# Kernel tuning notes

Measured on AMD Instinct MI355X. Metric: run time of the kernel, lower is better.

The kernel has to match this reference:

```python
import math
import jax, jax.numpy as jnp
import numpy as np

B, C, T = 2, 512, 2048
HEADS, NFREQS, NDECAY = 8, 4, 4
HD = C // HEADS  # head dim = 64


def _conv1x1(x, W, b):
    # pointwise Conv1d: W [out, in], b [out], x [B, in, T]
    return jnp.einsum('oi,bit->bot', W, x) + b[:, None]


def setup_inputs() -> dict:
    key = jax.random.key(0)
    ks = jax.random.split(key, 12)
    s = 1.0 / math.sqrt(C)
    inp = {
        'x': jax.random.normal(ks[0], (B, C, T), jnp.float32),
        'Wq': jax.random.normal(ks[1], (C, C), jnp.float32) * s,
        'bq': jnp.zeros((C,), jnp.float32),
        'Wk': jax.random.normal(ks[2], (C, C), jnp.float32) * s,
        'bk': jnp.zeros((C,), jnp.float32),
        'Wc': jax.random.normal(ks[3], (C, C), jnp.float32) * s,
        'bc': jnp.zeros((C,), jnp.float32),
        'Wqf': jax.random.normal(ks[4], (HEADS * NFREQS, C), jnp.float32) * s,
        'bqf': jnp.zeros((HEADS * NFREQS,), jnp.float32),
        # query_decay init: weight *= 0.01, bias = -2 (as in the torch module)
        'Wqd': jax.random.normal(ks[5], (HEADS * NDECAY, C), jnp.float32) * (s * 0.01),
        'bqd': jnp.full((HEADS * NDECAY,), -2.0, jnp.float32),
        'Wp': jax.random.normal(ks[6], (C, C), jnp.float32) * s,
        'bp': jnp.zeros((C,), jnp.float32),
    }
    return inp


def reference(x, Wq, bq, Wk, bk, Wc, bc, Wqf, bqf, Wqd, bqd, Wp, bp):
    Bx, Cx, Tx = x.shape
    idx = jnp.arange(Tx, dtype=x.dtype)
    delta = idx[:, None] - idx[None, :]  # [T, T]

    queries = _conv1x1(x, Wq, bq).reshape(Bx, HEADS, HD, Tx)
    keys = _conv1x1(x, Wk, bk).reshape(Bx, HEADS, HD, Tx)
    dots = jnp.einsum('bhct,bhcs->bhts', keys, queries) / math.sqrt(HD)

    # frequency bias
    periods = jnp.arange(1, NFREQS + 1, dtype=x.dtype)
    freq_kernel = jnp.cos(2 * math.pi * delta / periods[:, None, None])  # [f, T, T]
    freq_q = _conv1x1(x, Wqf, bqf).reshape(Bx, HEADS, NFREQS, Tx) / math.sqrt(NFREQS)
    dots = dots + jnp.einsum('fts,bhfs->bhts', freq_kernel, freq_q)

    # decay bias
    decays = jnp.arange(1, NDECAY + 1, dtype=x.dtype)
    decay_q = jax.nn.sigmoid(_conv1x1(x, Wqd, bqd).reshape(Bx, HEADS, NDECAY, Tx)) / 2
    decay_kernel = -decays[:, None, None] * jnp.abs(delta) / math.sqrt(NDECAY)
    dots = dots + jnp.einsum('fts,bhfs->bhts', decay_kernel, decay_q)

    # mask self-attention diagonal with -100, softmax over keys axis (t, dim=2)
    eye = jnp.eye(Tx, dtype=bool)
    dots = jnp.where(eye[None, None], jnp.asarray(-100.0, x.dtype), dots)
    weights = jax.nn.softmax(dots, axis=2)

    content = _conv1x1(x, Wc, bc).reshape(Bx, HEADS, HD, Tx)
    result = jnp.einsum('bhts,bhct->bhcs', weights, content).reshape(Bx, Cx, Tx)
    return x + _conv1x1(result, Wp, bp)
```

## Files before the change

kernel.cpp:

```cpp
#include <hip/hip_runtime.h>
#include <math.h>

#define T_SEQ 2048
#define C_DIM 512
#define B_SZ  2
#define NHEAD 8
#define HD    64
#define DP    128
#define MTOT  1600
#define NTILE 32

typedef unsigned short u16t;
typedef unsigned int   u32t;
typedef float f32x4 __attribute__((ext_vector_type(4)));
typedef short s16x8 __attribute__((ext_vector_type(8)));

__device__ __forceinline__ u32t pack2(float a, float b) {
    u32t r;
    asm("v_cvt_pk_bf16_f32 %0, %1, %2" : "=v"(r) : "v"(a), "v"(b));
    return r;
}
__device__ __forceinline__ u16t f2bf(float f) {
    union { float f; u32t u; } v; v.f = f;
    u32t r = v.u + 0x7fffu + ((v.u >> 16) & 1u);
    return (u16t)(r >> 16);
}
__device__ __forceinline__ float bf2f(u16t h) {
    union { u32t u; float f; } v; v.u = (u32t)h << 16; return v.f;
}

#define GLD16(g, l) __builtin_amdgcn_global_load_lds( \
    (const __attribute__((address_space(1))) u32t*)(g), \
    (__attribute__((address_space(3))) u32t*)(l), 16, 0, 0)

__global__ __launch_bounds__(256)
void wconv_kernel(const float* __restrict__ Wq, const float* __restrict__ Wk,
                  const float* __restrict__ Wc, const float* __restrict__ Wqf,
                  const float* __restrict__ Wqd, const float* __restrict__ Wp,
                  const float* __restrict__ bq, const float* __restrict__ bk,
                  const float* __restrict__ bc, const float* __restrict__ bqf,
                  const float* __restrict__ bqd,
                  u16t* __restrict__ Wcat, u16t* __restrict__ Wpbf,
                  float* __restrict__ biascat)
{
    int r = blockIdx.x, tid = threadIdx.x;
    if (r < MTOT) {
        const float* src;
        if (r < 512) src = Wq + (long long)r * C_DIM;
        else if (r < 1024) src = Wk + (long long)(r - 512) * C_DIM;
        else if (r < 1536) src = Wc + (long long)(r - 1024) * C_DIM;
        else if (r < 1568) src = Wqf + (long long)(r - 1536) * C_DIM;
        else src = Wqd + (long long)(r - 1568) * C_DIM;
        float2 v = *(const float2*)(src + tid * 2);
        *(u32t*)(Wcat + (long long)r * C_DIM + tid * 2) = pack2(v.x, v.y);
    } else if (r < MTOT + 512) {
        int rr = r - MTOT;
        float2 v = *(const float2*)(Wp + (long long)rr * C_DIM + tid * 2);
        *(u32t*)(Wpbf + (long long)rr * C_DIM + tid * 2) = pack2(v.x, v.y);
    } else {
        for (int i = tid; i < MTOT; i += 256) {
            float bv;
            if (i < 512) bv = bq[i];
            else if (i < 1024) bv = bk[i - 512];
            else if (i < 1536) bv = bc[i - 1024];
            else if (i < 1568) bv = bqf[i - 1536];
            else bv = bqd[i - 1568];
            biascat[i] = bv;
        }
    }
}

__global__ __launch_bounds__(256)
void xt_kernel(const float* __restrict__ x, u16t* __restrict__ xT)
{
    __shared__ float tile[64][65];
    int b = blockIdx.z, c0 = blockIdx.y * 64, t0 = blockIdx.x * 64;
    int tid = threadIdx.x;
    const float* xb = x + ((long long)b * C_DIM + c0) * T_SEQ + t0;
#pragma unroll
    for (int rr = 0; rr < 16; ++rr) {
        int row = rr * 4 + (tid >> 6);
        tile[row][tid & 63] = xb[(long long)row * T_SEQ + (tid & 63)];
    }
    __syncthreads();
    int tt = tid >> 2, cs = (tid & 3) * 16;
    u32t ov[8];
#pragma unroll
    for (int u = 0; u < 8; ++u)
        ov[u] = pack2(tile[cs + u * 2][tt], tile[cs + u * 2 + 1][tt]);
    u16t* dst = xT + ((long long)b * T_SEQ + t0 + tt) * C_DIM + c0 + cs;
    *(uint4*)(dst) = make_uint4(ov[0], ov[1], ov[2], ov[3]);
    *(uint4*)(dst + 8) = make_uint4(ov[4], ov[5], ov[6], ov[7]);
}

__global__ __launch_bounds__(256)
void gemm_kernel(const u16t* __restrict__ A, const u16t* __restrict__ Bm,
                 const float* __restrict__ biasv, const float* __restrict__ x,
                 u16t* __restrict__ Qbf, u16t* __restrict__ Kbf,
                 u16t* __restrict__ Vbf, float* __restrict__ fqd,
                 float* __restrict__ outp, int mode)
{
    __shared__ u16t At[2][64 * 64];
    __shared__ u16t Bt[2][64 * 64];
    int b = blockIdx.z, m0 = blockIdx.y * 64, n0 = blockIdx.x * 64;
    int tid = threadIdx.x, w = tid >> 6, lane = tid & 63;
    int l16 = lane & 15, l4 = lane >> 4;
    const u16t* Bb = Bm + (long long)b * T_SEQ * C_DIM;

    auto stage = [&](int kt, int bufi) {
        int k0 = kt * 64;
        const u16t* srcb = (w < 2) ? A + (long long)m0 * C_DIM + k0
                                   : Bb + (long long)n0 * C_DIM + k0;
        u16t* dstb = (w < 2) ? &At[bufi][0] : &Bt[bufi][0];
#pragma unroll
        for (int i = 0; i < 4; ++i) {
            int rb = (w & 1) * 32 + i * 8;
            int row = rb + (lane >> 3);
            int c = (lane & 7) ^ (row & 7);
            GLD16(srcb + (long long)row * C_DIM + c * 8, dstb + rb * 64);
        }
    };

    f32x4 acc[4] = {};
    stage(0, 0);
    for (int kt = 0; kt < 8; ++kt) {
        __syncthreads();
        if (kt < 7) stage(kt + 1, (kt + 1) & 1);
        const u16t* Ab = At[kt & 1];
        const u16t* Bb2 = Bt[kt & 1];
        int nl = w * 16 + l16;
#pragma unroll
        for (int kb = 0; kb < 2; ++kb) {
            s16x8 bf = *(const s16x8*)(&Bb2[nl * 64 + (((kb * 4 + l4) ^ (l16 & 7)) * 8)]);
#pragma unroll
            for (int rt = 0; rt < 4; ++rt) {
                s16x8 af = *(const s16x8*)(&At[kt & 1][(rt * 16 + l16) * 64 + (((kb * 4 + l4) ^ (l16 & 7)) * 8)]);
                acc[rt] = __builtin_amdgcn_mfma_f32_16x16x32_bf16(af, bf, acc[rt], 0, 0, 0);
            }
            (void)Ab;
        }
    }

    int n = n0 + w * 16 + l16;
    if (mode == 0) {
        if (m0 < 1024) {
            bool isQ = m0 < 512;
            int h = (isQ ? m0 : m0 - 512) >> 6;
            u16t* dst = (isQ ? Qbf : Kbf) + ((long long)(b * NHEAD + h) * T_SEQ + n) * DP;
            float sc = isQ ? 0.125f : 1.0f;
#pragma unroll
            for (int rt = 0; rt < 4; ++rt) {
                int d0 = (rt * 16 + l4 * 4) & 63;
                int m = m0 + rt * 16 + l4 * 4;
                float v0 = sc * (acc[rt][0] + biasv[m + 0]);
                float v1 = sc * (acc[rt][1] + biasv[m + 1]);
                float v2 = sc * (acc[rt][2] + biasv[m + 2]);
                float v3 = sc * (acc[rt][3] + biasv[m + 3]);
                *(uint2*)(dst + d0) = make_uint2(pack2(v0, v1), pack2(v2, v3));
            }
        } else if (m0 < 1536) {
#pragma unroll
            for (int rt = 0; rt < 4; ++rt)
#pragma unroll
                for (int j = 0; j < 4; ++j) {
                    int m = m0 + rt * 16 + l4 * 4 + j;
                    int c = m - 1024;
                    Vbf[((long long)b * C_DIM + c) * T_SEQ + n] = f2bf(acc[rt][j] + biasv[m]);
                }
        } else {
#pragma unroll
            for (int rt = 0; rt < 4; ++rt)
#pragma unroll
                for (int j = 0; j < 4; ++j) {
                    int m = m0 + rt * 16 + l4 * 4 + j;
                    fqd[((long long)b * 64 + (m - 1536)) * T_SEQ + n] = acc[rt][j] + biasv[m];
                }
        }
    } else {
#pragma unroll
        for (int rt = 0; rt < 4; ++rt)
#pragma unroll
            for (int j = 0; j < 4; ++j) {
                int m = m0 + rt * 16 + l4 * 4 + j;
                long long o = ((long long)b * C_DIM + m) * T_SEQ + n;
                outp[o] = acc[rt][j] + biasv[m] + x[o];
            }
    }
}

__global__ __launch_bounds__(256)
void kext_kernel(u16t* __restrict__ Kbf)
{
    int t = blockIdx.x * 256 + threadIdx.x;
    int bh = blockIdx.y;
    u32t e[4];
#pragma unroll
    for (int f = 0; f < 4; ++f) {
        float a = 2.0f * (float)t / (float)(f + 1);
        e[f] = pack2(cospif(a), sinpif(a));
    }
    u16t* row = Kbf + ((long long)bh * T_SEQ + t) * DP;
    *(uint4*)(row + 64) = make_uint4(e[0], e[1], e[2], e[3]);
    uint4 z = make_uint4(0, 0, 0, 0);
#pragma unroll
    for (int i = 0; i < 7; ++i) *(uint4*)(row + 72 + i * 8) = z;
}

__global__ __launch_bounds__(256)
void coef_kernel(const float* __restrict__ fqd, u16t* __restrict__ Qbf,
                 float* __restrict__ dcoef)
{
    int s = blockIdx.x * 256 + threadIdx.x;
    int bh = blockIdx.y, b = bh >> 3, h = bh & 7;
    const float* base = fqd + (long long)b * 64 * T_SEQ;
    float dsum = 0.f;
    u32t e[4];
#pragma unroll
    for (int f = 0; f < 4; ++f) {
        float fq = base[(long long)(h * 4 + f) * T_SEQ + s] * 0.5f;
        float zd = base[(long long)(32 + h * 4 + f) * T_SEQ + s];
        dsum += (float)(f + 1) / (1.f + __expf(-zd));
        float a = 2.0f * (float)s / (float)(f + 1);
        e[f] = pack2(fq * cospif(a), fq * sinpif(a));
    }
    u16t* row = Qbf + ((long long)bh * T_SEQ + s) * DP;
    *(uint4*)(row + 64) = make_uint4(e[0], e[1], e[2], e[3]);
    uint4 z = make_uint4(0, 0, 0, 0);
#pragma unroll
    for (int i = 0; i < 7; ++i) *(uint4*)(row + 72 + i * 8) = z;
    dcoef[(long long)bh * T_SEQ + s] = 0.25f * dsum;
}

__global__ __launch_bounds__(256)
void knorm_kernel(const u16t* __restrict__ Kbf, float* __restrict__ knorm)
{
    __shared__ float wmax[4];
    int tile = blockIdx.x, bh = blockIdx.y, tid = threadIdx.x;
    int row = tid >> 2, part = tid & 3;
    const u16t* rp = Kbf + ((long long)bh * T_SEQ + tile * 64 + row) * DP + part * 16;
    float ss = 0.f;
#pragma unroll
    for (int i = 0; i < 2; ++i) {
        s16x8 v = *(const s16x8*)(rp + i * 8);
#pragma unroll
        for (int e = 0; e < 8; ++e) { float f = bf2f((u16t)v[e]); ss += f * f; }
    }
    ss += __shfl_xor(ss, 1, 64);
    ss += __shfl_xor(ss, 2, 64);
    float nrm = sqrtf(ss + 4.1f);
#pragma unroll
    for (int off = 4; off < 64; off <<= 1) nrm = fmaxf(nrm, __shfl_xor(nrm, off, 64));
    if ((tid & 63) == 0) wmax[tid >> 6] = nrm;
    __syncthreads();
    if (tid == 0)
        knorm[bh * NTILE + tile] =
            fmaxf(fmaxf(wmax[0], wmax[1]), fmaxf(wmax[2], wmax[3]));
}

__global__ __launch_bounds__(256)
void attn_kernel(const u16t* __restrict__ Qbf, const u16t* __restrict__ Kbf,
                 const u16t* __restrict__ Vbf, const float* __restrict__ dcoef,
                 const float* __restrict__ knorm, u16t* __restrict__ Rt)
{
    __shared__ u16t Kt[2][64 * DP];
    __shared__ u16t Vt[2][64 * 64];
    __shared__ u16t Pl[4][16 * 64];
    __shared__ u32t voteLds[4];

    int bh = blockIdx.y, b = bh >> 3, h = bh & 7;
    int j0 = blockIdx.x;
    int s0 = j0 * 64;
    int tid = threadIdx.x, w = tid >> 6, lane = tid & 63;
    int l16 = lane & 15, l4 = lane >> 4;
    const u16t* Qg = Qbf + (long long)bh * T_SEQ * DP;
    const u16t* Kg = Kbf + (long long)bh * T_SEQ * DP;
    const u16t* Vg = Vbf + ((long long)b * C_DIM + h * HD) * T_SEQ;
    int sl = w * 16 + l16;
    int sg = s0 + sl;

    s16x8 qf[3];
#pragma unroll
    for (int kb = 0; kb < 3; ++kb)
        qf[kb] = *(const s16x8*)(Qg + (long long)sg * DP + kb * 32 + l4 * 8);
    float qn2 = 0.f;
#pragma unroll
    for (int kb = 0; kb < 3; ++kb)
#pragma unroll
        for (int e = 0; e < 8; ++e) { float f = bf2f((u16t)qf[kb][e]); qn2 += f * f; }
    qn2 += __shfl_xor(qn2, 16, 64);
    qn2 += __shfl_xor(qn2, 32, 64);
    float qn = sqrtf(qn2);
    float dc = dcoef[(long long)bh * T_SEQ + sg];
    float mrun = -1e30f, lrun = 0.f;
    f32x4 O4[4] = {};

    auto stageKV = [&](int tt0, int bufi) {
#pragma unroll
        for (int i = 0; i < 4; ++i) {
            int rb = w * 16 + i * 4;
            int row = rb + (lane >> 4);
            int c = (lane & 15) ^ (row & 7);
            GLD16(Kg + (long long)(tt0 + row) * DP + c * 8, &Kt[bufi][rb * DP]);
        }
#pragma unroll
        for (int i = 0; i < 2; ++i) {
            int cb = w * 16 + i * 8;
            int cc = cb + (lane >> 3);
            int tc = (lane & 7) ^ (cc & 7);
            GLD16(Vg + (long long)cc * T_SEQ + tt0 + tc * 8, &Vt[bufi][cb * 64]);
        }
    };

    auto compute_tile = [&](int tj, int bufi, bool diag) {
        const u16t* Kb = Kt[bufi];
        const u16t* Vb = Vt[bufi];
        int t0 = tj * 64;
        f32x4 sacc[4] = {};
#pragma unroll
        for (int kb = 0; kb < 3; ++kb)
#pragma unroll
            for (int rt = 0; rt < 4; ++rt) {
                s16x8 af = *(const s16x8*)(&Kb[(rt * 16 + l16) * DP + (((kb * 4 + l4) ^ (l16 & 7)) * 8)]);
                sacc[rt] = __builtin_amdgcn_mfma_f32_16x16x32_bf16(af, qf[kb], sacc[rt], 0, 0, 0);
            }
        float cm = mrun;
        float pv[4][4];
#pragma unroll
        for (int rt = 0; rt < 4; ++rt) {
            int tb = t0 + rt * 16 + l4 * 4;
#pragma unroll
            for (int j = 0; j < 4; ++j) {
                int t = tb + j;
                float v = sacc[rt][j] - fabsf((float)(t - sg)) * dc;
                if (diag && t == sg) v = -100.f;
                pv[rt][j] = v;
                cm = fmaxf(cm, v);
            }
        }
        cm = fmaxf(cm, __shfl_xor(cm, 16, 64));
        cm = fmaxf(cm, __shfl_xor(cm, 32, 64));
        if (__any(cm > mrun)) {
            float scale = __expf(mrun - cm);
            mrun = cm;
            lrun *= scale;
#pragma unroll
            for (int rt = 0; rt < 4; ++rt) O4[rt] *= scale;
        }
        float psum = 0.f;
#pragma unroll
        for (int rt = 0; rt < 4; ++rt)
#pragma unroll
            for (int j = 0; j < 4; ++j) {
                float p = __expf(pv[rt][j] - mrun);
                pv[rt][j] = p;
                psum += p;
            }
        psum += __shfl_xor(psum, 16, 64);
        psum += __shfl_xor(psum, 32, 64);
        lrun += psum;
#pragma unroll
        for (int rt = 0; rt < 4; ++rt) {
            int tl = rt * 16 + l4 * 4;
            int cp = (tl >> 3) ^ (l16 & 7);
            *(uint2*)(&Pl[w][l16 * 64 + cp * 8 + (tl & 7)]) =
                make_uint2(pack2(pv[rt][0], pv[rt][1]), pack2(pv[rt][2], pv[rt][3]));
        }
#pragma unroll
        for (int kb = 0; kb < 2; ++kb) {
            s16x8 pf = *(const s16x8*)(&Pl[w][l16 * 64 + (((kb * 4 + l4) ^ (l16 & 7)) * 8)]);
#pragma unroll
            for (int rt = 0; rt < 4; ++rt) {
                s16x8 vf = *(const s16x8*)(&Vb[(rt * 16 + l16) * 64 + (((kb * 4 + l4) ^ (l16 & 7)) * 8)]);
                O4[rt] = __builtin_amdgcn_mfma_f32_16x16x32_bf16(vf, pf, O4[rt], 0, 0, 0);
            }
        }
    };

    int seq[3]; int ns = 0;
    seq[ns++] = j0;
    if (j0 + 1 < NTILE) seq[ns++] = j0 + 1;
    if (j0 > 0) seq[ns++] = j0 - 1;
    stageKV(seq[0] * 64, 0);
    for (int i = 0; i < ns; ++i) {
        __syncthreads();
        if (i + 1 < ns) stageKV(seq[i + 1] * 64, (i + 1) & 1);
        compute_tile(seq[i], i & 1, seq[i] == j0);
    }

    u32t mask = 0;
    const float* knb = knorm + bh * NTILE;
    for (int j = 0; j < NTILE; ++j) {
        int d = j > j0 ? j - j0 : j0 - j;
        if (d <= 1) continue;
        float minD = (float)((d - 1) * 64 + 1);
        float bound = qn * knb[j] - dc * minD;
        if (__any(bound > mrun - 15.f)) mask |= 1u << j;
    }
    voteLds[w] = mask;
    __syncthreads();
    mask = voteLds[0] | voteLds[1] | voteLds[2] | voteLds[3];

    int parity = ns & 1;
    u32t rem = mask;
    if (rem) {
        int j = (int)__builtin_ctz(rem);
        stageKV(j * 64, parity);
        while (true) {
            rem &= rem - 1;
            __syncthreads();
            int nj = rem ? (int)__builtin_ctz(rem) : -1;
            if (nj >= 0) stageKV(nj * 64, parity ^ 1);
            compute_tile(j, parity, false);
            if (nj < 0) break;
            parity ^= 1;
            j = nj;
        }
    }

    __syncthreads();
    float inv = 1.f / lrun;
#pragma unroll
    for (int rt = 0; rt < 4; ++rt) {
        O4[rt] *= inv;
        int cb = rt * 16 + l4 * 4;
        int cp = (cb >> 3) ^ (sl & 7);
        *(uint2*)(&Kt[0][sl * 64 + cp * 8 + (cb & 7)]) =
            make_uint2(pack2(O4[rt][0], O4[rt][1]), pack2(O4[rt][2], O4[rt][3]));
    }
    __syncthreads();
    {
        int row = tid >> 2;
        int rsw = row & 7;
        u16t* dst = Rt + ((long long)b * T_SEQ + s0 + row) * C_DIM + h * HD;
#pragma unroll
        for (int i = 0; i < 2; ++i) {
            int cc = (tid & 3) + i * 4;
            uint4 v = *(const uint4*)(&Kt[0][row * 64 + ((cc ^ rsw) * 8)]);
            *(uint4*)(dst + cc * 8) = v;
        }
    }
}

extern "C" void kernel_launch(void* const* d_in, const int* in_sizes, int n_in,
                              void* d_out, int out_size, void* d_ws, size_t ws_size,
                              hipStream_t stream)
{
    const float* x   = (const float*)d_in[0];
    const float* Wq  = (const float*)d_in[1];
    const float* bq  = (const float*)d_in[2];
    const float* Wk  = (const float*)d_in[3];
    const float* bk  = (const float*)d_in[4];
    const float* Wc  = (const float*)d_in[5];
    const float* bc  = (const float*)d_in[6];
    const float* Wqf = (const float*)d_in[7];
    const float* bqf = (const float*)d_in[8];
    const float* Wqd = (const float*)d_in[9];
    const float* bqd = (const float*)d_in[10];
    const float* Wp  = (const float*)d_in[11];
    const float* bp  = (const float*)d_in[12];
    float* out = (float*)d_out;

    char* p = (char*)d_ws;
    u16t* Wcat = (u16t*)p;    p += (long long)MTOT * C_DIM * 2;
    u16t* Wpbf = (u16t*)p;    p += (long long)C_DIM * C_DIM * 2;
    float* biascat = (float*)p; p += MTOT * 4;
    u16t* xT = (u16t*)p;      p += (long long)B_SZ * T_SEQ * C_DIM * 2;
    u16t* Qbf = (u16t*)p;     p += (long long)16 * T_SEQ * DP * 2;
    u16t* Kbf = (u16t*)p;     p += (long long)16 * T_SEQ * DP * 2;
    u16t* Vbf = (u16t*)p;     p += (long long)B_SZ * C_DIM * T_SEQ * 2;
    float* fqd = (float*)p;   p += (long long)B_SZ * 64 * T_SEQ * 4;
    float* dcoef = (float*)p; p += (long long)16 * T_SEQ * 4;
    float* knorm = (float*)p; p += (long long)16 * NTILE * 4;
    u16t* Rt = (u16t*)p;      p += (long long)B_SZ * T_SEQ * C_DIM * 2;

    dim3 blk(256);
    hipLaunchKernelGGL(wconv_kernel, dim3(MTOT + 512 + 1), blk, 0, stream,
                       Wq, Wk, Wc, Wqf, Wqd, Wp, bq, bk, bc, bqf, bqd,
                       Wcat, Wpbf, biascat);
    hipLaunchKernelGGL(xt_kernel, dim3(T_SEQ / 64, C_DIM / 64, B_SZ), blk, 0, stream,
                       x, xT);
    hipLaunchKernelGGL(gemm_kernel, dim3(T_SEQ / 64, MTOT / 64, B_SZ), blk, 0, stream,
                       Wcat, xT, biascat, nullptr, Qbf, Kbf, Vbf, fqd, nullptr, 0);
    hipLaunchKernelGGL(kext_kernel, dim3(T_SEQ / 256, 16), blk, 0, stream, Kbf);
    hipLaunchKernelGGL(coef_kernel, dim3(T_SEQ / 256, 16), blk, 0, stream,
                       fqd, Qbf, dcoef);
    hipLaunchKernelGGL(knorm_kernel, dim3(NTILE, 16), blk, 0, stream, Kbf, knorm);
    hipLaunchKernelGGL(attn_kernel, dim3(T_SEQ / 64, 16), blk, 0, stream,
                       Qbf, Kbf, Vbf, dcoef, knorm, Rt);
    hipLaunchKernelGGL(gemm_kernel, dim3(T_SEQ / 64, C_DIM / 64, B_SZ), blk, 0, stream,
                       Wpbf, Rt, bp, (const float*)x, nullptr, nullptr, nullptr, nullptr,
                       out, 1);
}
```

Before: 63.78 us.

## Enlarge GEMM tiles, fuse Q/K extension kernels, add setprio and lazy softmax rescale

Replaces the 64x64 projection GEMM with a templated kernel that uses 128x128 tiles for the QKV/bias projection and 128x64 tiles for the output projection. Each wave now computes a 2D sub-tile, so every LDS fragment feeds more MFMAs, and the grid has fewer blocks. The last M tile overruns the 1600-row weight matrix, so its stores are guarded. The separate K-extension and coefficient kernels are merged into one launch that computes cos/sin once. The attention kernel gains s_setprio around its MFMA phases and rescales the online softmax only when the running max grows by more than 8, which trades some fp32 headroom for fewer rescale passes.

```diff
diff --git a/kernel.cpp b/kernel.cpp
--- a/kernel.cpp
+++ b/kernel.cpp
@@ -93,141 +93,165 @@
     *(uint4*)(dst + 8) = make_uint4(ov[4], ov[5], ov[6], ov[7]);
 }
 
+template<int BM, int BN, int MODE>
 __global__ __launch_bounds__(256)
-void gemm_kernel(const u16t* __restrict__ A, const u16t* __restrict__ Bm,
-                 const float* __restrict__ biasv, const float* __restrict__ x,
-                 u16t* __restrict__ Qbf, u16t* __restrict__ Kbf,
-                 u16t* __restrict__ Vbf, float* __restrict__ fqd,
-                 float* __restrict__ outp, int mode)
-{
-    __shared__ u16t At[2][64 * 64];
-    __shared__ u16t Bt[2][64 * 64];
-    int b = blockIdx.z, m0 = blockIdx.y * 64, n0 = blockIdx.x * 64;
+void gemm_big(const u16t* __restrict__ A, const u16t* __restrict__ Bm,
+              const float* __restrict__ biasv, const float* __restrict__ x,
+              u16t* __restrict__ Qbf, u16t* __restrict__ Kbf,
+              u16t* __restrict__ Vbf, float* __restrict__ fqd,
+              float* __restrict__ outp)
+{
+    constexpr int WM = BM / 2, WN = BN / 2, MT = WM / 16, NT = WN / 16;
+    __shared__ u16t At[2][BM * 64];
+    __shared__ u16t Bt[2][BN * 64];
+    int b = blockIdx.z, m0 = blockIdx.y * BM, n0 = blockIdx.x * BN;
     int tid = threadIdx.x, w = tid >> 6, lane = tid & 63;
+    int wy = w >> 1, wx = w & 1;
     int l16 = lane & 15, l4 = lane >> 4;
     const u16t* Bb = Bm + (long long)b * T_SEQ * C_DIM;
 
     auto stage = [&](int kt, int bufi) {
         int k0 = kt * 64;
-        const u16t* srcb = (w < 2) ? A + (long long)m0 * C_DIM + k0
-                                   : Bb + (long long)n0 * C_DIM + k0;
-        u16t* dstb = (w < 2) ? &At[bufi][0] : &Bt[bufi][0];
-#pragma unroll
-        for (int i = 0; i < 4; ++i) {
-            int rb = (w & 1) * 32 + i * 8;
+#pragma unroll
+        for (int i = 0; i < BM / 32; ++i) {
+            int rb = (w * (BM / 32) + i) * 8;
             int row = rb + (lane >> 3);
             int c = (lane & 7) ^ (row & 7);
-            GLD16(srcb + (long long)row * C_DIM + c * 8, dstb + rb * 64);
+            GLD16(A + (long long)(m0 + row) * C_DIM + k0 + c * 8, &At[bufi][rb * 64]);
+        }
+#pragma unroll
+        for (int i = 0; i < BN / 32; ++i) {
+            int rb = (w * (BN / 32) + i) * 8;
+            int row = rb + (lane >> 3);
+            int c = (lane & 7) ^ (row & 7);
+            GLD16(Bb + (long long)(n0 + row) * C_DIM + k0 + c * 8, &Bt[bufi][rb * 64]);
         }
     };
 
-    f32x4 acc[4] = {};
+    f32x4 acc[MT][NT] = {};
     stage(0, 0);
     for (int kt = 0; kt < 8; ++kt) {
         __syncthreads();
         if (kt < 7) stage(kt + 1, (kt + 1) & 1);
         const u16t* Ab = At[kt & 1];
         const u16t* Bb2 = Bt[kt & 1];
-        int nl = w * 16 + l16;
 #pragma unroll
         for (int kb = 0; kb < 2; ++kb) {
-            s16x8 bf = *(const s16x8*)(&Bb2[nl * 64 + (((kb * 4 + l4) ^ (l16 & 7)) * 8)]);
-#pragma unroll
-            for (int rt = 0; rt < 4; ++rt) {
-                s16x8 af = *(const s16x8*)(&At[kt & 1][(rt * 16 + l16) * 64 + (((kb * 4 + l4) ^ (l16 & 7)) * 8)]);
-                acc[rt] = __builtin_amdgcn_mfma_f32_16x16x32_bf16(af, bf, acc[rt], 0, 0, 0);
-            }
-            (void)Ab;
-        }
-    }
-
-    int n = n0 + w * 16 + l16;
-    if (mode == 0) {
-        if (m0 < 1024) {
-            bool isQ = m0 < 512;
-            int h = (isQ ? m0 : m0 - 512) >> 6;
-            u16t* dst = (isQ ? Qbf : Kbf) + ((long long)(b * NHEAD + h) * T_SEQ + n) * DP;
+            int co = ((kb * 4 + l4) ^ (l16 & 7)) * 8;
+            s16x8 bf[NT], af[MT];
+#pragma unroll
+            for (int nt = 0; nt < NT; ++nt)
+                bf[nt] = *(const s16x8*)(&Bb2[(wx * WN + nt * 16 + l16) * 64 + co]);
+#pragma unroll
+            for (int mt = 0; mt < MT; ++mt)
+                af[mt] = *(const s16x8*)(&Ab[(wy * WM + mt * 16 + l16) * 64 + co]);
+            __builtin_amdgcn_s_setprio(1);
+#pragma unroll
+            for (int mt = 0; mt < MT; ++mt)
+#pragma unroll
+                for (int nt = 0; nt < NT; ++nt)
+                    acc[mt][nt] = __builtin_amdgcn_mfma_f32_16x16x32_bf16(
+                        af[mt], bf[nt], acc[mt][nt], 0, 0, 0);
+            __builtin_amdgcn_s_setprio(0);
+        }
+    }
+
+    if (MODE == 0) {
+        int my = blockIdx.y;
+        if (my < 8) {
+            bool isQ = my < 4;
             float sc = isQ ? 0.125f : 1.0f;
 #pragma unroll
-            for (int rt = 0; rt < 4; ++rt) {
-                int d0 = (rt * 16 + l4 * 4) & 63;
-                int m = m0 + rt * 16 + l4 * 4;
-                float v0 = sc * (acc[rt][0] + biasv[m + 0]);
-                float v1 = sc * (acc[rt][1] + biasv[m + 1]);
-                float v2 = sc * (acc[rt][2] + biasv[m + 2]);
-                float v3 = sc * (acc[rt][3] + biasv[m + 3]);
-                *(uint2*)(dst + d0) = make_uint2(pack2(v0, v1), pack2(v2, v3));
-            }
-        } else if (m0 < 1536) {
-#pragma unroll
-            for (int rt = 0; rt < 4; ++rt)
+            for (int nt = 0; nt < NT; ++nt) {
+                int n = n0 + wx * WN + nt * 16 + l16;
+#pragma unroll
+                for (int mt = 0; mt < MT; ++mt) {
+                    int m = m0 + wy * WM + mt * 16 + l4 * 4;
+                    int idx = isQ ? m : m - 512;
+                    int h = idx >> 6, d0 = idx & 63;
+                    u16t* dst = (isQ ? Qbf : Kbf) +
+                        ((long long)(b * NHEAD + h) * T_SEQ + n) * DP + d0;
+                    float v0 = sc * (acc[mt][nt][0] + biasv[m + 0]);
+                    float v1 = sc * (acc[mt][nt][1] + biasv[m + 1]);
+                    float v2 = sc * (acc[mt][nt][2] + biasv[m + 2]);
+                    float v3 = sc * (acc[mt][nt][3] + biasv[m + 3]);
+                    *(uint2*)dst = make_uint2(pack2(v0, v1), pack2(v2, v3));
+                }
+            }
+        } else if (my < 12) {
+#pragma unroll
+            for (int nt = 0; nt < NT; ++nt) {
+                int n = n0 + wx * WN + nt * 16 + l16;
+#pragma unroll
+                for (int mt = 0; mt < MT; ++mt)
+#pragma unroll
+                    for (int j = 0; j < 4; ++j) {
+                        int m = m0 + wy * WM + mt * 16 + l4 * 4 + j;
+                        int c = m - 1024;
+                        Vbf[((long long)b * C_DIM + c) * T_SEQ + n] =
+                            f2bf(acc[mt][nt][j] + biasv[m]);
+                    }
+            }
+        } else {
+#pragma unroll
+            for (int nt = 0; nt < NT; ++nt) {
+                int n = n0 + wx * WN + nt * 16 + l16;
+#pragma unroll
+                for (int mt = 0; mt < MT; ++mt)
+#pragma unroll
+                    for (int j = 0; j < 4; ++j) {
+                        int m = m0 + wy * WM + mt * 16 + l4 * 4 + j;
+                        int r = m - 1536;
+                        if (r < 64)
+                            fqd[((long long)b * 64 + r) * T_SEQ + n] =
+                                acc[mt][nt][j] + biasv[m];
+                    }
+            }
+        }
+    } else {
+#pragma unroll
+        for (int nt = 0; nt < NT; ++nt) {
+            int n = n0 + wx * WN + nt * 16 + l16;
+#pragma unroll
+            for (int mt = 0; mt < MT; ++mt)
 #pragma unroll
                 for (int j = 0; j < 4; ++j) {
-                    int m = m0 + rt * 16 + l4 * 4 + j;
-                    int c = m - 1024;
-                    Vbf[((long long)b * C_DIM + c) * T_SEQ + n] = f2bf(acc[rt][j] + biasv[m]);
+                    int m = m0 + wy * WM + mt * 16 + l4 * 4 + j;
+                    long long o = ((long long)b * C_DIM + m) * T_SEQ + n;
+                    outp[o] = acc[mt][nt][j] + biasv[m] + x[o];
                 }
-        } else {
-#pragma unroll
-            for (int rt = 0; rt < 4; ++rt)
-#pragma unroll
-                for (int j = 0; j < 4; ++j) {
-                    int m = m0 + rt * 16 + l4 * 4 + j;
-                    fqd[((long long)b * 64 + (m - 1536)) * T_SEQ + n] = acc[rt][j] + biasv[m];
-                }
-        }
-    } else {
-#pragma unroll
-        for (int rt = 0; rt < 4; ++rt)
-#pragma unroll
-            for (int j = 0; j < 4; ++j) {
-                int m = m0 + rt * 16 + l4 * 4 + j;
-                long long o = ((long long)b * C_DIM + m) * T_SEQ + n;
-                outp[o] = acc[rt][j] + biasv[m] + x[o];
-            }
+        }
     }
 }
 
 __global__ __launch_bounds__(256)
-void kext_kernel(u16t* __restrict__ Kbf)
-{
-    int t = blockIdx.x * 256 + threadIdx.x;
-    int bh = blockIdx.y;
-    u32t e[4];
-#pragma unroll
-    for (int f = 0; f < 4; ++f) {
-        float a = 2.0f * (float)t / (float)(f + 1);
-        e[f] = pack2(cospif(a), sinpif(a));
-    }
-    u16t* row = Kbf + ((long long)bh * T_SEQ + t) * DP;
-    *(uint4*)(row + 64) = make_uint4(e[0], e[1], e[2], e[3]);
-    uint4 z = make_uint4(0, 0, 0, 0);
-#pragma unroll
-    for (int i = 0; i < 7; ++i) *(uint4*)(row + 72 + i * 8) = z;
-}
-
-__global__ __launch_bounds__(256)
-void coef_kernel(const float* __restrict__ fqd, u16t* __restrict__ Qbf,
-                 float* __restrict__ dcoef)
+void ext_kernel(const float* __restrict__ fqd, u16t* __restrict__ Qbf,
+                u16t* __restrict__ Kbf, float* __restrict__ dcoef)
 {
     int s = blockIdx.x * 256 + threadIdx.x;
     int bh = blockIdx.y, b = bh >> 3, h = bh & 7;
     const float* base = fqd + (long long)b * 64 * T_SEQ;
     float dsum = 0.f;
-    u32t e[4];
+    u32t eq[4], ek[4];
 #pragma unroll
     for (int f = 0; f < 4; ++f) {
         float fq = base[(long long)(h * 4 + f) * T_SEQ + s] * 0.5f;
         float zd = base[(long long)(32 + h * 4 + f) * T_SEQ + s];
         dsum += (float)(f + 1) / (1.f + __expf(-zd));
         float a = 2.0f * (float)s / (float)(f + 1);
-        e[f] = pack2(fq * cospif(a), fq * sinpif(a));
-    }
-    u16t* row = Qbf + ((long long)bh * T_SEQ + s) * DP;
-    *(uint4*)(row + 64) = make_uint4(e[0], e[1], e[2], e[3]);
+        float cv = cospif(a), sv = sinpif(a);
+        ek[f] = pack2(cv, sv);
+        eq[f] = pack2(fq * cv, fq * sv);
+    }
     uint4 z = make_uint4(0, 0, 0, 0);
-#pragma unroll
-    for (int i = 0; i < 7; ++i) *(uint4*)(row + 72 + i * 8) = z;
+    u16t* qrow = Qbf + ((long long)bh * T_SEQ + s) * DP;
+    *(uint4*)(qrow + 64) = make_uint4(eq[0], eq[1], eq[2], eq[3]);
+#pragma unroll
+    for (int i = 0; i < 7; ++i) *(uint4*)(qrow + 72 + i * 8) = z;
+    u16t* krow = Kbf + ((long long)bh * T_SEQ + s) * DP;
+    *(uint4*)(krow + 64) = make_uint4(ek[0], ek[1], ek[2], ek[3]);
+#pragma unroll
+    for (int i = 0; i < 7; ++i) *(uint4*)(krow + 72 + i * 8) = z;
     dcoef[(long long)bh * T_SEQ + s] = 0.25f * dsum;
 }
 
@@ -316,6 +340,7 @@
         const u16t* Vb = Vt[bufi];
         int t0 = tj * 64;
         f32x4 sacc[4] = {};
+        __builtin_amdgcn_s_setprio(1);
 #pragma unroll
         for (int kb = 0; kb < 3; ++kb)
 #pragma unroll
@@ -323,6 +348,7 @@
                 s16x8 af = *(const s16x8*)(&Kb[(rt * 16 + l16) * DP + (((kb * 4 + l4) ^ (l16 & 7)) * 8)]);
                 sacc[rt] = __builtin_amdgcn_mfma_f32_16x16x32_bf16(af, qf[kb], sacc[rt], 0, 0, 0);
             }
+        __builtin_amdgcn_s_setprio(0);
         float cm = mrun;
         float pv[4][4];
 #pragma unroll
@@ -339,7 +365,7 @@
         }
         cm = fmaxf(cm, __shfl_xor(cm, 16, 64));
         cm = fmaxf(cm, __shfl_xor(cm, 32, 64));
-        if (__any(cm > mrun)) {
+        if (!__all(cm - mrun <= 8.f)) {
             float scale = __expf(mrun - cm);
             mrun = cm;
             lrun *= scale;
@@ -365,6 +391,7 @@
             *(uint2*)(&Pl[w][l16 * 64 + cp * 8 + (tl & 7)]) =
                 make_uint2(pack2(pv[rt][0], pv[rt][1]), pack2(pv[rt][2], pv[rt][3]));
         }
+        __builtin_amdgcn_s_setprio(1);
 #pragma unroll
         for (int kb = 0; kb < 2; ++kb) {
             s16x8 pf = *(const s16x8*)(&Pl[w][l16 * 64 + (((kb * 4 + l4) ^ (l16 & 7)) * 8)]);
@@ -374,6 +401,7 @@
                 O4[rt] = __builtin_amdgcn_mfma_f32_16x16x32_bf16(vf, pf, O4[rt], 0, 0, 0);
             }
         }
+        __builtin_amdgcn_s_setprio(0);
     };
 
     int seq[3]; int ns = 0;
@@ -479,15 +507,14 @@
                        Wcat, Wpbf, biascat);
     hipLaunchKernelGGL(xt_kernel, dim3(T_SEQ / 64, C_DIM / 64, B_SZ), blk, 0, stream,
                        x, xT);
-    hipLaunchKernelGGL(gemm_kernel, dim3(T_SEQ / 64, MTOT / 64, B_SZ), blk, 0, stream,
-                       Wcat, xT, biascat, nullptr, Qbf, Kbf, Vbf, fqd, nullptr, 0);
-    hipLaunchKernelGGL(kext_kernel, dim3(T_SEQ / 256, 16), blk, 0, stream, Kbf);
-    hipLaunchKernelGGL(coef_kernel, dim3(T_SEQ / 256, 16), blk, 0, stream,
-                       fqd, Qbf, dcoef);
+    hipLaunchKernelGGL((gemm_big<128, 128, 0>), dim3(T_SEQ / 128, 13, B_SZ), blk, 0,
+                       stream, Wcat, xT, biascat, nullptr, Qbf, Kbf, Vbf, fqd, nullptr);
+    hipLaunchKernelGGL(ext_kernel, dim3(T_SEQ / 256, 16), blk, 0, stream,
+                       fqd, Qbf, Kbf, dcoef);
     hipLaunchKernelGGL(knorm_kernel, dim3(NTILE, 16), blk, 0, stream, Kbf, knorm);
     hipLaunchKernelGGL(attn_kernel, dim3(T_SEQ / 64, 16), blk, 0, stream,
                        Qbf, Kbf, Vbf, dcoef, knorm, Rt);
-    hipLaunchKernelGGL(gemm_kernel, dim3(T_SEQ / 64, C_DIM / 64, B_SZ), blk, 0, stream,
-                       Wpbf, Rt, bp, (const float*)x, nullptr, nullptr, nullptr, nullptr,
-                       out, 1);
-}
+    hipLaunchKernelGGL((gemm_big<128, 64, 1>), dim3(T_SEQ / 64, C_DIM / 128, B_SZ),
+                       blk, 0, stream, Wpbf, Rt, bp, x, nullptr, nullptr,
+                       nullptr, nullptr, out);
+}
```

Result: slower. 69.68 us (+9.2%).
